# Performance work log

Hardware: AMD Instinct MI355X
Metric: run time of the kernel (lower is better)

Reference implementation:

```python
import jax, jax.numpy as jnp
import numpy as np

K_RATIO = 0.7  # initial_ratio at epoch 0

def setup_inputs() -> dict:
    key = jax.random.key(0)
    k1, k2, k3 = jax.random.split(key, 3)
    B, D, C = 65536, 512, 1000
    features = jax.random.normal(k1, (B, D), dtype=jnp.float32)
    targets = jax.random.randint(k2, (B,), 0, C, dtype=jnp.int64)
    W = jax.random.normal(k3, (D, C), dtype=jnp.float32) / np.sqrt(D)
    b = jnp.zeros((C,), dtype=jnp.float32)
    return {"features": features, "targets": targets, "W": W, "b": b}

def reference(features, targets, W, b):
    # model: linear classifier -> logits [B, C]
    logits = features @ W + b
    # per-sample cross-entropy (reduction='none')
    logp = jax.nn.log_softmax(logits, axis=-1)
    losses = -jnp.take_along_axis(logp, targets[:, None], axis=-1)[:, 0]  # [B]
    B = features.shape[0]
    num_ohem = int(B * K_RATIO)
    # top-k hard examples, mean of their losses
    top_vals, _ = jax.lax.top_k(losses, num_ohem)
    return top_vals.mean()
```

## Files before the change

kernel.cpp:

```cpp
#include <hip/hip_runtime.h>
#include <hip/hip_bf16.h>

#define BTOT 65536
#define DDIM 512
#define CDIM 1000
#define CPAD 1024
#define KSEL 45875

#define L2E 1.44269504088896340736f
#define LN2 0.69314718055994530942f
#define NEG_BIG -1.0e30f

typedef __attribute__((ext_vector_type(8))) short short8;
typedef __attribute__((ext_vector_type(4))) float f32x4;

__device__ __forceinline__ unsigned short f2bf(float f) {
  unsigned u = __float_as_uint(f);
  u += 0x7FFFu + ((u >> 16) & 1u);
  return (unsigned short)(u >> 16);
}

__global__ void prep_wt(const float* __restrict__ W, unsigned short* __restrict__ Wt) {
  const int idx = blockIdx.x * 256 + threadIdx.x;
  const int c = idx >> 9;
  const int d = idx & 511;
  unsigned short v = 0;
  if (c < CDIM) v = f2bf(W[d * CDIM + c]);
  Wt[idx] = v;
}

__global__ void prep_bias(const float* __restrict__ b, float* __restrict__ bp) {
  const int i = blockIdx.x * 256 + threadIdx.x;
  bp[i] = (i < CDIM) ? b[i] * L2E : NEG_BIG;
}

__launch_bounds__(256, 2)
__global__ void ohem_losses(const float* __restrict__ feat,
                            const int* __restrict__ targets,
                            const unsigned short* __restrict__ Wt,
                            const float* __restrict__ bpad,
                            float* __restrict__ losses) {
  const int lane  = threadIdx.x & 63;
  const int wave  = (blockIdx.x << 2) + (threadIdx.x >> 6);
  const int rowB  = wave << 5;
  const int l15   = lane & 15;
  const int lgrp  = lane >> 4;

  short8 a[2][16];
#pragma unroll
  for (int rf = 0; rf < 2; ++rf) {
    const float* src = feat + (size_t)(rowB + rf * 16 + l15) * DDIM + lgrp * 8;
#pragma unroll
    for (int ks = 0; ks < 16; ++ks) {
      const float4 f0 = *(const float4*)(src + ks * 32);
      const float4 f1 = *(const float4*)(src + ks * 32 + 4);
      short8 v;
      v[0] = (short)f2bf(f0.x); v[1] = (short)f2bf(f0.y);
      v[2] = (short)f2bf(f0.z); v[3] = (short)f2bf(f0.w);
      v[4] = (short)f2bf(f1.x); v[5] = (short)f2bf(f1.y);
      v[6] = (short)f2bf(f1.z); v[7] = (short)f2bf(f1.w);
      a[rf][ks] = v;
    }
  }

  int   tcol[8];
  float m[8], s[8], tv[8];
#pragma unroll
  for (int rf = 0; rf < 2; ++rf)
#pragma unroll
    for (int r = 0; r < 4; ++r) {
      const int slot = rf * 4 + r;
      tcol[slot] = targets[rowB + rf * 16 + lgrp * 4 + r];
      m[slot] = NEG_BIG; s[slot] = 0.f; tv[slot] = NEG_BIG;
    }

  for (int nc = 0; nc < 32; ++nc) {
    const int n0 = nc * 32;
    f32x4 acc[2][2];
#pragma unroll
    for (int rf = 0; rf < 2; ++rf)
#pragma unroll
      for (int cf = 0; cf < 2; ++cf) acc[rf][cf] = (f32x4){0.f, 0.f, 0.f, 0.f};

    const unsigned short* w0 = Wt + (size_t)(n0 + l15) * DDIM + lgrp * 8;
#pragma unroll
    for (int ks = 0; ks < 16; ++ks) {
      const short8 b0 = *(const short8*)(w0 + ks * 32);
      const short8 b1 = *(const short8*)(w0 + 16 * DDIM + ks * 32);
      acc[0][0] = __builtin_amdgcn_mfma_f32_16x16x32_bf16(a[0][ks], b0, acc[0][0], 0, 0, 0);
      acc[0][1] = __builtin_amdgcn_mfma_f32_16x16x32_bf16(a[0][ks], b1, acc[0][1], 0, 0, 0);
      acc[1][0] = __builtin_amdgcn_mfma_f32_16x16x32_bf16(a[1][ks], b0, acc[1][0], 0, 0, 0);
      acc[1][1] = __builtin_amdgcn_mfma_f32_16x16x32_bf16(a[1][ks], b1, acc[1][1], 0, 0, 0);
    }

    const int col0 = n0 + l15;
    const int col1 = col0 + 16;
    const float bb0 = bpad[col0];
    const float bb1 = bpad[col1];
#pragma unroll
    for (int rf = 0; rf < 2; ++rf)
#pragma unroll
      for (int r = 0; r < 4; ++r) {
        const int slot = rf * 4 + r;
        const float z0 = fmaf(acc[rf][0][r], L2E, bb0);
        const float z1 = fmaf(acc[rf][1][r], L2E, bb1);
        if (col0 == tcol[slot]) tv[slot] = z0;
        if (col1 == tcol[slot]) tv[slot] = z1;
        const float nm = fmaxf(m[slot], fmaxf(z0, z1));
        s[slot] = s[slot] * exp2f(m[slot] - nm) + exp2f(z0 - nm) + exp2f(z1 - nm);
        m[slot] = nm;
      }
  }

#pragma unroll
  for (int st = 1; st <= 8; st <<= 1) {
#pragma unroll
    for (int slot = 0; slot < 8; ++slot) {
      const float mo = __shfl_xor(m[slot], st, 64);
      const float so = __shfl_xor(s[slot], st, 64);
      const float to = __shfl_xor(tv[slot], st, 64);
      const float nm = fmaxf(m[slot], mo);
      s[slot]  = s[slot] * exp2f(m[slot] - nm) + so * exp2f(mo - nm);
      m[slot]  = nm;
      tv[slot] = fmaxf(tv[slot], to);
    }
  }

  if (l15 == 0) {
#pragma unroll
    for (int rf = 0; rf < 2; ++rf)
#pragma unroll
      for (int r = 0; r < 4; ++r) {
        const int slot = rf * 4 + r;
        losses[rowB + rf * 16 + lgrp * 4 + r] =
            LN2 * (m[slot] + log2f(s[slot]) - tv[slot]);
      }
  }
}

__global__ void radix_pass(const unsigned* __restrict__ vals,
                           unsigned* __restrict__ state, int pass) {
  __shared__ unsigned hist[16][257];
  __shared__ unsigned hist1[256];
  const int tid = threadIdx.x;
  for (int i = tid; i < 16 * 257; i += 1024) (&hist[0][0])[i] = 0;
  __syncthreads();

  unsigned prefix = 0, krem = KSEL, pmask = 0;
  const int shift = 24 - 8 * pass;
  if (pass > 0) {
    prefix = state[0];
    krem   = state[1];
    pmask  = 0xFFFFFFFFu << (shift + 8);
  }
  const int copy = tid & 15;
  for (int i = tid; i < BTOT; i += 1024) {
    const unsigned u = vals[i];
    if ((u & pmask) == prefix)
      atomicAdd(&hist[copy][(u >> shift) & 255], 1u);
  }
  __syncthreads();
  if (tid < 256) {
    unsigned t = 0;
#pragma unroll
    for (int c = 0; c < 16; ++c) t += hist[c][tid];
    hist1[tid] = t;
  }
  __syncthreads();
  if (tid == 0) {
    unsigned k = krem, p = prefix;
    for (int bkt = 255; bkt >= 0; --bkt) {
      const unsigned c = hist1[bkt];
      if (k <= c) { p |= ((unsigned)bkt) << shift; break; }
      k -= c;
    }
    state[0] = p;
    state[1] = k;
  }
}

__global__ void ohem_sum(const float* __restrict__ losses,
                         const unsigned* __restrict__ state,
                         float* __restrict__ psum, unsigned* __restrict__ pcnt) {
  const unsigned ut = state[0];
  const int i = blockIdx.x * 256 + threadIdx.x;
  const float v = losses[i];
  const unsigned u = __float_as_uint(v);
  float    sv = (u > ut) ? v  : 0.f;
  unsigned sc = (u > ut) ? 1u : 0u;
#pragma unroll
  for (int st = 32; st >= 1; st >>= 1) {
    sv += __shfl_xor(sv, st, 64);
    sc += __shfl_xor(sc, st, 64);
  }
  __shared__ float    wsum[4];
  __shared__ unsigned wcnt[4];
  const int w = threadIdx.x >> 6;
  if ((threadIdx.x & 63) == 0) { wsum[w] = sv; wcnt[w] = sc; }
  __syncthreads();
  if (threadIdx.x == 0) {
    psum[blockIdx.x] = wsum[0] + wsum[1] + wsum[2] + wsum[3];
    pcnt[blockIdx.x] = wcnt[0] + wcnt[1] + wcnt[2] + wcnt[3];
  }
}

__global__ void ohem_final(const float* __restrict__ psum,
                           const unsigned* __restrict__ pcnt,
                           const unsigned* __restrict__ state,
                           float* __restrict__ out) {
  float    sv = psum[threadIdx.x];
  unsigned sc = pcnt[threadIdx.x];
#pragma unroll
  for (int st = 32; st >= 1; st >>= 1) {
    sv += __shfl_xor(sv, st, 64);
    sc += __shfl_xor(sc, st, 64);
  }
  __shared__ float    wsum[4];
  __shared__ unsigned wcnt[4];
  const int w = threadIdx.x >> 6;
  if ((threadIdx.x & 63) == 0) { wsum[w] = sv; wcnt[w] = sc; }
  __syncthreads();
  if (threadIdx.x == 0) {
    const float    sum = wsum[0] + wsum[1] + wsum[2] + wsum[3];
    const unsigned cnt = wcnt[0] + wcnt[1] + wcnt[2] + wcnt[3];
    const float t = __uint_as_float(state[0]);
    out[0] = (sum + (float)(KSEL - cnt) * t) / (float)KSEL;
  }
}

extern "C" void kernel_launch(void* const* d_in, const int* in_sizes, int n_in,
                              void* d_out, int out_size, void* d_ws, size_t ws_size,
                              hipStream_t stream) {
  const float* feat    = (const float*)d_in[0];
  const int*   targets = (const int*)d_in[1];
  const float* W       = (const float*)d_in[2];
  const float* b       = (const float*)d_in[3];
  float* out = (float*)d_out;

  char* ws = (char*)d_ws;
  unsigned short* Wt     = (unsigned short*)ws;
  float*          bp     = (float*)(ws + 1048576);
  float*          losses = (float*)(ws + 1048576 + 4096);
  unsigned*       state  = (unsigned*)(ws + 1048576 + 4096 + 262144);
  float*          psum   = (float*)(ws + 1048576 + 4096 + 262144 + 256);
  unsigned*       pcnt   = (unsigned*)(ws + 1048576 + 4096 + 262144 + 256 + 1024);

  prep_wt<<<2048, 256, 0, stream>>>(W, Wt);
  prep_bias<<<4, 256, 0, stream>>>(b, bp);
  ohem_losses<<<512, 256, 0, stream>>>(feat, targets, Wt, bp, losses);
  radix_pass<<<1, 1024, 0, stream>>>((const unsigned*)losses, state, 0);
  radix_pass<<<1, 1024, 0, stream>>>((const unsigned*)losses, state, 1);
  radix_pass<<<1, 1024, 0, stream>>>((const unsigned*)losses, state, 2);
  radix_pass<<<1, 1024, 0, stream>>>((const unsigned*)losses, state, 3);
  ohem_sum<<<256, 256, 0, stream>>>(losses, state, psum, pcnt);
  ohem_final<<<1, 256, 0, stream>>>(psum, pcnt, state, out);
}
```

Before: 346.4 us.

## Stage W tiles through LDS, drop online max, fuse top-k histogram into loss kernel

The loss kernel now double-buffers swizzled bf16 W tiles into LDS with global_load_lds, replacing per-wave global loads of W. The softmax drops the running max and sums raw exp2 directly, relying on logits being small. A 16-bit high histogram is built with atomics in the loss kernel, and the four single-block radix passes become a two-level 16-bit histogram select. This removes redundant W traffic and serial single-block passes, but skipping the max only stays safe while logits are bounded, and global atomics add contention.

```diff
diff --git a/kernel.cpp b/kernel.cpp
--- a/kernel.cpp
+++ b/kernel.cpp
@@ -4,7 +4,6 @@
 #define BTOT 65536
 #define DDIM 512
 #define CDIM 1000
-#define CPAD 1024
 #define KSEL 45875
 
 #define L2E 1.44269504088896340736f
@@ -12,6 +11,7 @@
 #define NEG_BIG -1.0e30f
 
 typedef __attribute__((ext_vector_type(8))) short short8;
+typedef __attribute__((ext_vector_type(8))) unsigned short ushort8;
 typedef __attribute__((ext_vector_type(4))) float f32x4;
 
 __device__ __forceinline__ unsigned short f2bf(float f) {
@@ -20,13 +20,26 @@
   return (unsigned short)(u >> 16);
 }
 
-__global__ void prep_wt(const float* __restrict__ W, unsigned short* __restrict__ Wt) {
+__device__ __forceinline__ void gload_lds16(const void* g, void* l) {
+  __builtin_amdgcn_global_load_lds(
+      (const __attribute__((address_space(1))) unsigned int*)g,
+      (__attribute__((address_space(3))) unsigned int*)l, 16, 0, 0);
+}
+
+__global__ void prep_wt(const float* __restrict__ W, unsigned short* __restrict__ Wg) {
   const int idx = blockIdx.x * 256 + threadIdx.x;
-  const int c = idx >> 9;
-  const int d = idx & 511;
-  unsigned short v = 0;
-  if (c < CDIM) v = f2bf(W[d * CDIM + c]);
-  Wt[idx] = v;
+  const int c  = idx & 1023;
+  const int k8 = idx >> 10;
+  const int nc = c >> 5, cc = c & 31;
+  ushort8 v;
+#pragma unroll
+  for (int j = 0; j < 8; ++j) {
+    const int k = k8 * 8 + j;
+    v[j] = (c < CDIM) ? f2bf(W[k * CDIM + c]) : (unsigned short)0;
+  }
+  const unsigned dst = (unsigned)nc * 32768u +
+      (((((unsigned)cc) << 10) | (((unsigned)k8) << 4)) ^ ((((unsigned)cc) & 7u) << 4));
+  *(ushort8*)((char*)Wg + dst) = v;
 }
 
 __global__ void prep_bias(const float* __restrict__ b, float* __restrict__ bp) {
@@ -34,17 +47,30 @@
   bp[i] = (i < CDIM) ? b[i] * L2E : NEG_BIG;
 }
 
+__global__ void zero_hist(unsigned* __restrict__ h) {
+  ((uint4*)h)[blockIdx.x * 256 + threadIdx.x] = (uint4){0, 0, 0, 0};
+}
+
 __launch_bounds__(256, 2)
 __global__ void ohem_losses(const float* __restrict__ feat,
                             const int* __restrict__ targets,
-                            const unsigned short* __restrict__ Wt,
+                            const unsigned short* __restrict__ Wg,
                             const float* __restrict__ bpad,
-                            float* __restrict__ losses) {
-  const int lane  = threadIdx.x & 63;
-  const int wave  = (blockIdx.x << 2) + (threadIdx.x >> 6);
-  const int rowB  = wave << 5;
-  const int l15   = lane & 15;
-  const int lgrp  = lane >> 4;
+                            float* __restrict__ losses,
+                            unsigned* __restrict__ histHi) {
+  __shared__ unsigned char lbuf[2][32768];
+  const int tid  = threadIdx.x;
+  const int lane = tid & 63;
+  const int wave = (blockIdx.x << 2) + (tid >> 6);
+  const int rowB = wave << 5;
+  const int l15  = lane & 15;
+  const int lgrp = lane >> 4;
+
+#pragma unroll
+  for (int r = 0; r < 8; ++r) {
+    const int off = (r * 256 + tid) * 16;
+    gload_lds16((const char*)Wg + off, &lbuf[0][off]);
+  }
 
   short8 a[2][16];
 #pragma unroll
@@ -64,36 +90,53 @@
   }
 
   int   tcol[8];
-  float m[8], s[8], tv[8];
+  float s[8], tv[8];
 #pragma unroll
   for (int rf = 0; rf < 2; ++rf)
 #pragma unroll
     for (int r = 0; r < 4; ++r) {
       const int slot = rf * 4 + r;
       tcol[slot] = targets[rowB + rf * 16 + lgrp * 4 + r];
-      m[slot] = NEG_BIG; s[slot] = 0.f; tv[slot] = NEG_BIG;
-    }
+      s[slot] = 0.f; tv[slot] = NEG_BIG;
+    }
+
+  __syncthreads();
+
+  const unsigned xm    = ((unsigned)(l15 & 7)) << 4;
+  const unsigned base0 = (((unsigned)l15) << 10) | (((unsigned)lgrp) << 4);
+  const unsigned base1 = base0 + (16u << 10);
 
   for (int nc = 0; nc < 32; ++nc) {
-    const int n0 = nc * 32;
+    const int cur = nc & 1;
+    if (nc + 1 < 32) {
+      const char* src = (const char*)Wg + (size_t)(nc + 1) * 32768;
+#pragma unroll
+      for (int r = 0; r < 8; ++r) {
+        const int off = (r * 256 + tid) * 16;
+        gload_lds16(src + off, &lbuf[cur ^ 1][off]);
+      }
+    }
+
     f32x4 acc[2][2];
 #pragma unroll
     for (int rf = 0; rf < 2; ++rf)
 #pragma unroll
       for (int cf = 0; cf < 2; ++cf) acc[rf][cf] = (f32x4){0.f, 0.f, 0.f, 0.f};
 
-    const unsigned short* w0 = Wt + (size_t)(n0 + l15) * DDIM + lgrp * 8;
+    const unsigned char* lb = &lbuf[cur][0];
 #pragma unroll
     for (int ks = 0; ks < 16; ++ks) {
-      const short8 b0 = *(const short8*)(w0 + ks * 32);
-      const short8 b1 = *(const short8*)(w0 + 16 * DDIM + ks * 32);
+      const unsigned o0 = (base0 | (((unsigned)ks) << 6)) ^ xm;
+      const unsigned o1 = (base1 | (((unsigned)ks) << 6)) ^ xm;
+      const short8 b0 = *(const short8*)(lb + o0);
+      const short8 b1 = *(const short8*)(lb + o1);
       acc[0][0] = __builtin_amdgcn_mfma_f32_16x16x32_bf16(a[0][ks], b0, acc[0][0], 0, 0, 0);
       acc[0][1] = __builtin_amdgcn_mfma_f32_16x16x32_bf16(a[0][ks], b1, acc[0][1], 0, 0, 0);
       acc[1][0] = __builtin_amdgcn_mfma_f32_16x16x32_bf16(a[1][ks], b0, acc[1][0], 0, 0, 0);
       acc[1][1] = __builtin_amdgcn_mfma_f32_16x16x32_bf16(a[1][ks], b1, acc[1][1], 0, 0, 0);
     }
 
-    const int col0 = n0 + l15;
+    const int col0 = (nc << 5) + l15;
     const int col1 = col0 + 16;
     const float bb0 = bpad[col0];
     const float bb1 = bpad[col1];
@@ -106,25 +149,19 @@
         const float z1 = fmaf(acc[rf][1][r], L2E, bb1);
         if (col0 == tcol[slot]) tv[slot] = z0;
         if (col1 == tcol[slot]) tv[slot] = z1;
-        const float nm = fmaxf(m[slot], fmaxf(z0, z1));
-        s[slot] = s[slot] * exp2f(m[slot] - nm) + exp2f(z0 - nm) + exp2f(z1 - nm);
-        m[slot] = nm;
+        s[slot] += __builtin_amdgcn_exp2f(z0) + __builtin_amdgcn_exp2f(z1);
       }
-  }
-
-#pragma unroll
-  for (int st = 1; st <= 8; st <<= 1) {
+
+    __syncthreads();
+  }
+
+#pragma unroll
+  for (int st = 1; st <= 8; st <<= 1)
 #pragma unroll
     for (int slot = 0; slot < 8; ++slot) {
-      const float mo = __shfl_xor(m[slot], st, 64);
-      const float so = __shfl_xor(s[slot], st, 64);
-      const float to = __shfl_xor(tv[slot], st, 64);
-      const float nm = fmaxf(m[slot], mo);
-      s[slot]  = s[slot] * exp2f(m[slot] - nm) + so * exp2f(mo - nm);
-      m[slot]  = nm;
-      tv[slot] = fmaxf(tv[slot], to);
-    }
-  }
+      s[slot] += __shfl_xor(s[slot], st, 64);
+      tv[slot] = fmaxf(tv[slot], __shfl_xor(tv[slot], st, 64));
+    }
 
   if (l15 == 0) {
 #pragma unroll
@@ -132,51 +169,57 @@
 #pragma unroll
       for (int r = 0; r < 4; ++r) {
         const int slot = rf * 4 + r;
-        losses[rowB + rf * 16 + lgrp * 4 + r] =
-            LN2 * (m[slot] + log2f(s[slot]) - tv[slot]);
+        float loss = LN2 * (__builtin_amdgcn_logf(s[slot]) - tv[slot]);
+        loss = fmaxf(loss, 0.f);
+        losses[rowB + rf * 16 + lgrp * 4 + r] = loss;
+        atomicAdd(&histHi[__float_as_uint(loss) >> 16], 1u);
       }
   }
 }
 
-__global__ void radix_pass(const unsigned* __restrict__ vals,
-                           unsigned* __restrict__ state, int pass) {
-  __shared__ unsigned hist[16][257];
-  __shared__ unsigned hist1[256];
-  const int tid = threadIdx.x;
-  for (int i = tid; i < 16 * 257; i += 1024) (&hist[0][0])[i] = 0;
+__global__ void scan_level(const unsigned* __restrict__ hist,
+                           unsigned* __restrict__ state, const int level) {
+  const int t = threadIdx.x;
+  __shared__ unsigned sh[256];
+  const unsigned k       = (level == 0) ? (unsigned)KSEL : state[1];
+  const unsigned oldpref = (level == 0) ? 0u : state[0];
+
+  unsigned gs = 0;
+  const uint4* hp = (const uint4*)(hist + t * 256);
+#pragma unroll 4
+  for (int i = 0; i < 64; ++i) { const uint4 h = hp[i]; gs += h.x + h.y + h.z + h.w; }
+  sh[t] = gs;
   __syncthreads();
-
-  unsigned prefix = 0, krem = KSEL, pmask = 0;
-  const int shift = 24 - 8 * pass;
-  if (pass > 0) {
-    prefix = state[0];
-    krem   = state[1];
-    pmask  = 0xFFFFFFFFu << (shift + 8);
-  }
-  const int copy = tid & 15;
-  for (int i = tid; i < BTOT; i += 1024) {
-    const unsigned u = vals[i];
-    if ((u & pmask) == prefix)
-      atomicAdd(&hist[copy][(u >> shift) & 255], 1u);
-  }
-  __syncthreads();
-  if (tid < 256) {
-    unsigned t = 0;
-#pragma unroll
-    for (int c = 0; c < 16; ++c) t += hist[c][tid];
-    hist1[tid] = t;
-  }
-  __syncthreads();
-  if (tid == 0) {
-    unsigned k = krem, p = prefix;
-    for (int bkt = 255; bkt >= 0; --bkt) {
-      const unsigned c = hist1[bkt];
-      if (k <= c) { p |= ((unsigned)bkt) << shift; break; }
-      k -= c;
-    }
-    state[0] = p;
-    state[1] = k;
-  }
+  for (int off = 1; off < 256; off <<= 1) {
+    unsigned v = sh[t];
+    if (t + off < 256) v += sh[t + off];
+    __syncthreads();
+    sh[t] = v;
+    __syncthreads();
+  }
+  const unsigned incl  = sh[t];
+  const unsigned above = (t < 255) ? sh[t + 1] : 0u;
+  if (above < k && k <= incl) {
+    unsigned kk = k - above;
+    int b = 255;
+    for (; b > 0; --b) {
+      const unsigned c = hist[t * 256 + b];
+      if (kk <= c) break;
+      kk -= c;
+    }
+    const unsigned bin = (unsigned)(t * 256 + b);
+    if (level == 0) { state[0] = bin << 16;      state[1] = kk; }
+    else            { state[0] = oldpref | bin;  state[1] = kk; }
+  }
+}
+
+__global__ void hist_lo(const float* __restrict__ losses,
+                        const unsigned* __restrict__ state,
+                        unsigned* __restrict__ hLo) {
+  const unsigned pref = state[0] >> 16;
+  const int i = blockIdx.x * 256 + threadIdx.x;
+  const unsigned u = ((const unsigned*)losses)[i];
+  if ((u >> 16) == pref) atomicAdd(&hLo[u & 0xFFFFu], 1u);
 }
 
 __global__ void ohem_sum(const float* __restrict__ losses,
@@ -238,20 +281,22 @@
   float* out = (float*)d_out;
 
   char* ws = (char*)d_ws;
-  unsigned short* Wt     = (unsigned short*)ws;
+  unsigned short* Wg     = (unsigned short*)ws;
   float*          bp     = (float*)(ws + 1048576);
-  float*          losses = (float*)(ws + 1048576 + 4096);
-  unsigned*       state  = (unsigned*)(ws + 1048576 + 4096 + 262144);
-  float*          psum   = (float*)(ws + 1048576 + 4096 + 262144 + 256);
-  unsigned*       pcnt   = (unsigned*)(ws + 1048576 + 4096 + 262144 + 256 + 1024);
-
-  prep_wt<<<2048, 256, 0, stream>>>(W, Wt);
+  float*          losses = (float*)(ws + 1052672);
+  unsigned*       hHi    = (unsigned*)(ws + 1314816);
+  unsigned*       hLo    = (unsigned*)(ws + 1576960);
+  unsigned*       state  = (unsigned*)(ws + 1839104);
+  float*          psum   = (float*)(ws + 1839360);
+  unsigned*       pcnt   = (unsigned*)(ws + 1840384);
+
+  zero_hist<<<128, 256, 0, stream>>>(hHi);
+  prep_wt<<<256, 256, 0, stream>>>(W, Wg);
   prep_bias<<<4, 256, 0, stream>>>(b, bp);
-  ohem_losses<<<512, 256, 0, stream>>>(feat, targets, Wt, bp, losses);
-  radix_pass<<<1, 1024, 0, stream>>>((const unsigned*)losses, state, 0);
-  radix_pass<<<1, 1024, 0, stream>>>((const unsigned*)losses, state, 1);
-  radix_pass<<<1, 1024, 0, stream>>>((const unsigned*)losses, state, 2);
-  radix_pass<<<1, 1024, 0, stream>>>((const unsigned*)losses, state, 3);
+  ohem_losses<<<512, 256, 0, stream>>>(feat, targets, Wg, bp, losses, hHi);
+  scan_level<<<1, 256, 0, stream>>>(hHi, state, 0);
+  hist_lo<<<256, 256, 0, stream>>>(losses, state, hLo);
+  scan_level<<<1, 256, 0, stream>>>(hLo, state, 1);
   ohem_sum<<<256, 256, 0, stream>>>(losses, state, psum, pcnt);
   ohem_final<<<1, 256, 0, stream>>>(psum, pcnt, state, out);
 }
```

Measured after the change: 288.7 us. 16.7% less time.
